# Kernel optimization log

Measured on AMD Instinct MI355X. Metric: run time of the kernel, lower is better.

The kernel has to match this reference:

```python
import jax, jax.numpy as jnp
import numpy as np

INPUT, HIDDEN = 128, 64
B, T = 512, 1024


def _lstm_dir(x, Wih, Whh, b):
    """Single-direction LSTM (PyTorch gate order i,f,g,o). x: [B,T,I] -> [B,T,H]."""
    Bn = x.shape[0]
    H = Whh.shape[1]
    # precompute input contributions for all timesteps: [B,T,4H]
    xg = jnp.einsum('bti,gi->btg', x, Wih) + b

    def step(carry, g_t):
        h, c = carry
        g = g_t + h @ Whh.T  # [B,4H]
        i, f, gg, o = jnp.split(g, 4, axis=-1)
        c = jax.nn.sigmoid(f) * c + jax.nn.sigmoid(i) * jnp.tanh(gg)
        h = jax.nn.sigmoid(o) * jnp.tanh(c)
        return (h, c), h

    h0 = jnp.zeros((Bn, H), x.dtype)
    (_, _), hs = jax.lax.scan(step, (h0, h0), jnp.swapaxes(xg, 0, 1))
    return jnp.swapaxes(hs, 0, 1)  # [B,T,H]


def setup_inputs() -> dict:
    key = jax.random.key(0)
    ks = jax.random.split(key, 9)
    s_ih = 1.0 / np.sqrt(HIDDEN)
    def u(k, shape):
        return jax.random.uniform(k, shape, jnp.float32, -s_ih, s_ih)
    return {
        'x': jax.random.normal(ks[0], (B, T, INPUT), jnp.float32),
        'Wih_f': u(ks[1], (4 * HIDDEN, INPUT)),
        'Whh_f': u(ks[2], (4 * HIDDEN, HIDDEN)),
        'b_f': u(ks[3], (4 * HIDDEN,)),   # b_ih + b_hh folded (same math)
        'Wih_b': u(ks[4], (4 * HIDDEN, INPUT)),
        'Whh_b': u(ks[5], (4 * HIDDEN, HIDDEN)),
        'b_b': u(ks[6], (4 * HIDDEN,)),
    }


def reference(x, Wih_f, Whh_f, b_f, Wih_b, Whh_b, b_b):
    # forward returns the full bidirectional sequence output [B,T,2H]
    out_f = _lstm_dir(x, Wih_f, Whh_f, b_f)
    out_b = _lstm_dir(x[:, ::-1], Wih_b, Whh_b, b_b)[:, ::-1]
    return jnp.concatenate([out_f, out_b], axis=-1)
```

## Files before the change

kernel.cpp:

```cpp
#include <hip/hip_runtime.h>

#define T_LEN 1024
#define IN_DIM 128
#define HID 64

typedef __attribute__((ext_vector_type(8))) short short8;
typedef __attribute__((ext_vector_type(4))) float floatx4;
typedef __attribute__((ext_vector_type(2))) float floatx2;

__device__ __forceinline__ unsigned short f2bf(float v) {
    union { float f; unsigned u; } a; a.f = v;
    unsigned r = a.u + 0x7FFFu + ((a.u >> 16) & 1u);
    return (unsigned short)(r >> 16);
}

__device__ __forceinline__ short8 cvt8(const float* p) {
    short8 r;
#pragma unroll
    for (int j = 0; j < 8; ++j) r[j] = (short)f2bf(p[j]);
    return r;
}

#define LOG2E 1.44269504088896f
__device__ __forceinline__ float sigm(float x) {
    return __builtin_amdgcn_rcpf(1.0f + __builtin_amdgcn_exp2f(x * -LOG2E));
}
__device__ __forceinline__ float tanh_(float x) {
    return 2.0f * __builtin_amdgcn_rcpf(1.0f + __builtin_amdgcn_exp2f(x * -2.0f * LOG2E)) - 1.0f;
}

__global__ __launch_bounds__(256, 1) void lstm_bidir(
    const float* __restrict__ x,
    const float* __restrict__ WihF, const float* __restrict__ WhhF, const float* __restrict__ bF,
    const float* __restrict__ WihB, const float* __restrict__ WhhB, const float* __restrict__ bB,
    float* __restrict__ out)
{
    const int tid  = threadIdx.x;
    const int w    = tid >> 6;
    const int lane = tid & 63;
    const int nloc = lane & 15;
    const int quad = lane >> 4;
    const int bid  = blockIdx.x;
    const int dir  = bid & 1;
    const int b0   = (bid >> 1) * 4;

    const float* Wih  = dir ? WihB : WihF;
    const float* Whh  = dir ? WhhB : WhhF;
    const float* bias = dir ? bB   : bF;

    __shared__ unsigned short x_s[2][4 * 136];
    __shared__ unsigned short h_s[2][4 * 72];

    for (int i = tid; i < 2 * 4 * 72; i += 256) ((unsigned short*)h_s)[i] = 0;

    short8 wihf[4][4];
    short8 whhf[4][2];
    float  bv[4];
#pragma unroll
    for (int gc = 0; gc < 4; ++gc) {
        const int row = gc * 64 + w * 16 + nloc;
        bv[gc] = bias[row];
#pragma unroll
        for (int kf = 0; kf < 4; ++kf)
            wihf[gc][kf] = cvt8(Wih + row * IN_DIM + kf * 32 + quad * 8);
#pragma unroll
        for (int kf = 0; kf < 2; ++kf)
            whhf[gc][kf] = cvt8(Whh + row * HID + kf * 32 + quad * 8);
    }

    const int sr = tid >> 6;
    const int sk = (tid & 63) * 2;
    const float* xrow = x + (size_t)(b0 + sr) * T_LEN * IN_DIM + sk;

    auto tmap = [&](int s) {
        int ss = s < T_LEN - 1 ? s : T_LEN - 1;
        return dir ? (T_LEN - 1 - ss) : ss;
    };

    {
        floatx2 v = *(const floatx2*)(xrow + (size_t)tmap(0) * IN_DIM);
        unsigned pack = (unsigned)f2bf(v.x) | ((unsigned)f2bf(v.y) << 16);
        *(unsigned*)&x_s[0][sr * 136 + sk] = pack;
    }
    floatx2 pfA = *(const floatx2*)(xrow + (size_t)tmap(1) * IN_DIM);
    floatx2 pfB;

    float c = 0.f;

    __syncthreads();

    float* outcol = out + ((size_t)(b0 + quad) * T_LEN) * 128 + dir * HID + w * 16 + nloc;

    auto step = [&](int t, floatx2& useReg, floatx2& loadReg) {
        const int buf = t & 1;

        loadReg = *(const floatx2*)(xrow + (size_t)tmap(t + 2) * IN_DIM);

        short8 xa[4], ha[2];
        const unsigned short* xb = &x_s[buf][(nloc >> 2) * 136 + quad * 8];
#pragma unroll
        for (int kf = 0; kf < 4; ++kf) xa[kf] = *(const short8*)(xb + kf * 32);
        const unsigned short* hb = &h_s[buf][(nloc >> 2) * 72 + quad * 8];
#pragma unroll
        for (int kf = 0; kf < 2; ++kf) ha[kf] = *(const short8*)(hb + kf * 32);

        floatx4 acc[4];
#pragma unroll
        for (int gc = 0; gc < 4; ++gc) acc[gc] = (floatx4){bv[gc], bv[gc], bv[gc], bv[gc]};
#pragma unroll
        for (int kf = 0; kf < 4; ++kf)
#pragma unroll
            for (int gc = 0; gc < 4; ++gc)
                acc[gc] = __builtin_amdgcn_mfma_f32_16x16x32_bf16(xa[kf], wihf[gc][kf], acc[gc], 0, 0, 0);
#pragma unroll
        for (int kf = 0; kf < 2; ++kf)
#pragma unroll
            for (int gc = 0; gc < 4; ++gc)
                acc[gc] = __builtin_amdgcn_mfma_f32_16x16x32_bf16(ha[kf], whhf[gc][kf], acc[gc], 0, 0, 0);

        const int tg = tmap(t);
        {
            float iv = sigm(acc[0][0]);
            float fv = sigm(acc[1][0]);
            float gv = tanh_(acc[2][0]);
            float ov = sigm(acc[3][0]);
            c = fv * c + iv * gv;
            float hv = ov * tanh_(c);
            outcol[(size_t)tg * 128] = hv;
            h_s[buf ^ 1][quad * 72 + w * 16 + nloc] = f2bf(hv);
        }
        {
            unsigned pack = (unsigned)f2bf(useReg.x) | ((unsigned)f2bf(useReg.y) << 16);
            *(unsigned*)&x_s[buf ^ 1][sr * 136 + sk] = pack;
        }
        __syncthreads();
    };

    for (int t = 0; t < T_LEN; t += 2) {
        step(t, pfA, pfB);
        step(t + 1, pfB, pfA);
    }
}

extern "C" void kernel_launch(void* const* d_in, const int* in_sizes, int n_in,
                              void* d_out, int out_size, void* d_ws, size_t ws_size,
                              hipStream_t stream) {
    const float* x    = (const float*)d_in[0];
    const float* WihF = (const float*)d_in[1];
    const float* WhhF = (const float*)d_in[2];
    const float* bF   = (const float*)d_in[3];
    const float* WihB = (const float*)d_in[4];
    const float* WhhB = (const float*)d_in[5];
    const float* bB   = (const float*)d_in[6];
    float* out = (float*)d_out;

    lstm_bidir<<<dim3(256), dim3(256), 0, stream>>>(x, WihF, WhhF, bF, WihB, WhhB, bB, out);
}
```

Before: 871.1 us.

## Software-pipeline input projection one step ahead of recurrent matmul

The x·Wih MFMA contribution for step t+1 is now computed during step t. Each step's critical path before the gate nonlinearities then holds only the two recurrent h·Whh MFMAs, and the input-projection MFMAs can overlap with the activations. The x prefetch is deepened to four steps with two staged LDS buffers, and the LDS row strides are changed to 160/96. This costs extra accumulator registers and a more intricate buffer rotation that could be mis-indexed.

After: 835.6 us. 1.04x faster.

```diff
diff --git a/kernel.cpp b/kernel.cpp
--- a/kernel.cpp
+++ b/kernel.cpp
@@ -3,6 +3,8 @@
 #define T_LEN 1024
 #define IN_DIM 128
 #define HID 64
+#define XSTR 160
+#define HSTR 96
 
 typedef __attribute__((ext_vector_type(8))) short short8;
 typedef __attribute__((ext_vector_type(4))) float floatx4;
@@ -29,6 +31,7 @@
     return 2.0f * __builtin_amdgcn_rcpf(1.0f + __builtin_amdgcn_exp2f(x * -2.0f * LOG2E)) - 1.0f;
 }
 
+
 __global__ __launch_bounds__(256, 1) void lstm_bidir(
     const float* __restrict__ x,
     const float* __restrict__ WihF, const float* __restrict__ WhhF, const float* __restrict__ bF,
@@ -48,10 +51,10 @@
     const float* Whh  = dir ? WhhB : WhhF;
     const float* bias = dir ? bB   : bF;
 
-    __shared__ unsigned short x_s[2][4 * 136];
-    __shared__ unsigned short h_s[2][4 * 72];
+    __shared__ unsigned short x_s[2][4 * XSTR];
+    __shared__ unsigned short h_s[2][4 * HSTR];
 
-    for (int i = tid; i < 2 * 4 * 72; i += 256) ((unsigned short*)h_s)[i] = 0;
+    for (int i = tid; i < 2 * 4 * HSTR; i += 256) ((unsigned short*)h_s)[i] = 0;
 
     short8 wihf[4][4];
     short8 whhf[4][2];
@@ -77,46 +80,67 @@
         return dir ? (T_LEN - 1 - ss) : ss;
     };
 
-    {
-        floatx2 v = *(const floatx2*)(xrow + (size_t)tmap(0) * IN_DIM);
+    auto stage = [&](int s, int buf) {
+        floatx2 v = *(const floatx2*)(xrow + (size_t)tmap(s) * IN_DIM);
         unsigned pack = (unsigned)f2bf(v.x) | ((unsigned)f2bf(v.y) << 16);
-        *(unsigned*)&x_s[0][sr * 136 + sk] = pack;
-    }
-    floatx2 pfA = *(const floatx2*)(xrow + (size_t)tmap(1) * IN_DIM);
-    floatx2 pfB;
+        *(unsigned*)&x_s[buf][sr * XSTR + sk] = pack;
+    };
+    stage(0, 0);
+    stage(1, 1);
+    floatx2 pfA = *(const floatx2*)(xrow + (size_t)tmap(2) * IN_DIM);
+    floatx2 pfB = *(const floatx2*)(xrow + (size_t)tmap(3) * IN_DIM);
 
     float c = 0.f;
 
     __syncthreads();
 
-    float* outcol = out + ((size_t)(b0 + quad) * T_LEN) * 128 + dir * HID + w * 16 + nloc;
-
-    auto step = [&](int t, floatx2& useReg, floatx2& loadReg) {
-        const int buf = t & 1;
-
-        loadReg = *(const floatx2*)(xrow + (size_t)tmap(t + 2) * IN_DIM);
-
-        short8 xa[4], ha[2];
-        const unsigned short* xb = &x_s[buf][(nloc >> 2) * 136 + quad * 8];
+    floatx4 xacc0[4], xacc1[4];
+    {
+        short8 xa[4];
+        const unsigned short* xb = &x_s[0][(nloc >> 2) * XSTR + quad * 8];
 #pragma unroll
         for (int kf = 0; kf < 4; ++kf) xa[kf] = *(const short8*)(xb + kf * 32);
-        const unsigned short* hb = &h_s[buf][(nloc >> 2) * 72 + quad * 8];
+        __syncthreads();
 #pragma unroll
-        for (int kf = 0; kf < 2; ++kf) ha[kf] = *(const short8*)(hb + kf * 32);
-
-        floatx4 acc[4];
-#pragma unroll
-        for (int gc = 0; gc < 4; ++gc) acc[gc] = (floatx4){bv[gc], bv[gc], bv[gc], bv[gc]};
+        for (int gc = 0; gc < 4; ++gc) xacc0[gc] = (floatx4){bv[gc], bv[gc], bv[gc], bv[gc]};
 #pragma unroll
         for (int kf = 0; kf < 4; ++kf)
 #pragma unroll
             for (int gc = 0; gc < 4; ++gc)
-                acc[gc] = __builtin_amdgcn_mfma_f32_16x16x32_bf16(xa[kf], wihf[gc][kf], acc[gc], 0, 0, 0);
+                xacc0[gc] = __builtin_amdgcn_mfma_f32_16x16x32_bf16(xa[kf], wihf[gc][kf], xacc0[gc], 0, 0, 0);
+    }
+
+    float* outcol = out + ((size_t)(b0 + quad) * T_LEN) * 128 + dir * HID + w * 16 + nloc;
+
+    auto step = [&](int t, int cur, floatx4* xaccC, floatx4* xaccN, floatx2& pf) {
+        floatx2 old = pf;
+        pf = *(const floatx2*)(xrow + (size_t)tmap(t + 4) * IN_DIM);
+
+        short8 ha[2];
+        const unsigned short* hb = &h_s[cur][(nloc >> 2) * HSTR + quad * 8];
 #pragma unroll
-        for (int kf = 0; kf < 2; ++kf)
+        for (int kf = 0; kf < 2; ++kf) ha[kf] = *(const short8*)(hb + kf * 32);
+
+        short8 xa[4];
+        const unsigned short* xb = &x_s[cur ^ 1][(nloc >> 2) * XSTR + quad * 8];
+#pragma unroll
+        for (int kf = 0; kf < 4; ++kf) xa[kf] = *(const short8*)(xb + kf * 32);
+
+        floatx4 acc[4];
+#pragma unroll
+        for (int gc = 0; gc < 4; ++gc)
+            acc[gc] = __builtin_amdgcn_mfma_f32_16x16x32_bf16(ha[0], whhf[gc][0], xaccC[gc], 0, 0, 0);
+#pragma unroll
+        for (int gc = 0; gc < 4; ++gc)
+            acc[gc] = __builtin_amdgcn_mfma_f32_16x16x32_bf16(ha[1], whhf[gc][1], acc[gc], 0, 0, 0);
+
+#pragma unroll
+        for (int gc = 0; gc < 4; ++gc) xaccN[gc] = (floatx4){bv[gc], bv[gc], bv[gc], bv[gc]};
+#pragma unroll
+        for (int kf = 0; kf < 4; ++kf)
 #pragma unroll
             for (int gc = 0; gc < 4; ++gc)
-                acc[gc] = __builtin_amdgcn_mfma_f32_16x16x32_bf16(ha[kf], whhf[gc][kf], acc[gc], 0, 0, 0);
+                xaccN[gc] = __builtin_amdgcn_mfma_f32_16x16x32_bf16(xa[kf], wihf[gc][kf], xaccN[gc], 0, 0, 0);
 
         const int tg = tmap(t);
         {
@@ -127,18 +151,18 @@
             c = fv * c + iv * gv;
             float hv = ov * tanh_(c);
             outcol[(size_t)tg * 128] = hv;
-            h_s[buf ^ 1][quad * 72 + w * 16 + nloc] = f2bf(hv);
+            h_s[cur ^ 1][quad * HSTR + w * 16 + nloc] = f2bf(hv);
         }
         {
-            unsigned pack = (unsigned)f2bf(useReg.x) | ((unsigned)f2bf(useReg.y) << 16);
-            *(unsigned*)&x_s[buf ^ 1][sr * 136 + sk] = pack;
+            unsigned pack = (unsigned)f2bf(old.x) | ((unsigned)f2bf(old.y) << 16);
+            *(unsigned*)&x_s[cur][sr * XSTR + sk] = pack;
         }
         __syncthreads();
     };
 
     for (int t = 0; t < T_LEN; t += 2) {
-        step(t, pfA, pfB);
-        step(t + 1, pfB, pfA);
+        step(t,     0, xacc0, xacc1, pfA);
+        step(t + 1, 1, xacc1, xacc0, pfB);
     }
 }
 
```
